# Performance work log

Measured on AMD Instinct MI355X. Metric: run time of the kernel, lower is better.

Reference implementation:

```python
import jax, jax.numpy as jnp
import numpy as np

B, FIN, FOUT, N_TASKS = 256, 1024, 512, 20
FOUT2 = 2 * FOUT  # ConditionalLinear is built with 2*fout


def setup_inputs() -> dict:
    key = jax.random.key(0)
    k1, k2, k3 = jax.random.split(key, 3)
    x = jax.random.normal(k1, (B, FIN), dtype=jnp.float32)
    task_id = jax.random.randint(k2, (B,), 0, N_TASKS)
    # Embedding table [n_tasks, fin*2*fout]; kaiming_normal(fan_out) std = sqrt(2/fout2)
    std = np.sqrt(2.0 / FOUT2).astype(np.float32)
    W = jax.random.normal(k3, (N_TASKS, FIN * FOUT2), dtype=jnp.float32) * std
    return {"x": x, "task_id": task_id, "W": W}


def reference(x, task_id, W):
    Bsz, fin = x.shape
    fout2 = W.shape[1] // fin
    # task-conditional weight gather: [B, 2*fout, fin]
    w = W[task_id].reshape(Bsz, fout2, fin)
    # per-sample matvec (torch.bmm with x.unsqueeze(2))
    logits = jnp.einsum('boi,bi->bo', w, x).reshape(Bsz, fout2 // 2, 2)
    # BinaryGumbelSoftmax eval path: h = 1 - argmax(softmax(logits)) = 1 - argmax(logits)
    h = 1.0 - jnp.argmax(logits, axis=-1).astype(logits.dtype)
    return (h, logits)
```

## Files before the change

kernel.cpp:

```cpp
#include <hip/hip_runtime.h>

#define FIN   1024
#define FOUT2 1024
#define NTASK 20
#define BSZ   256
#define HOFF  (256 * 512)

__global__ __launch_bounds__(256, 2)
void cond_linear_kernel(const float* __restrict__ x,
                        const int* __restrict__ task_id,
                        const float* __restrict__ W,
                        float* __restrict__ out) {
    __shared__ int sh_ord[BSZ];
    __shared__ int wcnt[4];
    __shared__ int sh_n;

    const int tid  = threadIdx.x;
    const int lane = tid & 63;
    const int wv   = tid >> 6;
    const int t    = blockIdx.x >> 6;
    const int tile = blockIdx.x & 63;
    const int o0   = tile * 16 + wv * 4;

    const int my_task = task_id[tid];
    const bool match = (my_task == t);
    const unsigned long long m64 = __ballot(match);
    if (lane == 0) wcnt[wv] = __popcll(m64);
    __syncthreads();
    int base = 0;
    #pragma unroll
    for (int w = 0; w < 4; ++w)
        if (w < wv) base += wcnt[w];
    if (match) {
        const int pos = base + __popcll(m64 & ((1ull << lane) - 1ull));
        sh_ord[pos] = tid;
    }
    if (tid == 0) sh_n = wcnt[0] + wcnt[1] + wcnt[2] + wcnt[3];
    __syncthreads();
    const int n = sh_n;
    if (n == 0) return;

    const float* Wt = W + (size_t)t * (FOUT2 * FIN);
    float4 wr[4][4];
    #pragma unroll
    for (int r = 0; r < 4; ++r) {
        const float4* wp = (const float4*)(Wt + (size_t)(o0 + r) * FIN);
        #pragma unroll
        for (int p = 0; p < 4; ++p)
            wr[r][p] = wp[p * 64 + lane];
    }
    #pragma unroll
    for (int r = 0; r < 4; ++r)
        #pragma unroll
        for (int p = 0; p < 4; ++p)
            asm volatile("" : "+v"(wr[r][p].x), "+v"(wr[r][p].y),
                              "+v"(wr[r][p].z), "+v"(wr[r][p].w));

    int sa = sh_ord[0];
    int sb = sh_ord[(n > 1) ? 1 : 0];
    float4 xa[4], xb[4];
    #pragma unroll
    for (int p = 0; p < 4; ++p)
        xa[p] = ((const float4*)(x + (size_t)sa * FIN))[p * 64 + lane];
    #pragma unroll
    for (int p = 0; p < 4; ++p)
        xb[p] = ((const float4*)(x + (size_t)sb * FIN))[p * 64 + lane];

    for (int i = 0; i + 1 < n; i += 2) {
        const int ia2 = (i + 2 < n) ? i + 2 : i;
        const int ib2 = (i + 3 < n) ? i + 3 : ia2;
        const int na_s = sh_ord[ia2];
        const int nb_s = sh_ord[ib2];
        float4 na[4], nb[4];
        #pragma unroll
        for (int p = 0; p < 4; ++p)
            na[p] = ((const float4*)(x + (size_t)na_s * FIN))[p * 64 + lane];
        #pragma unroll
        for (int p = 0; p < 4; ++p)
            nb[p] = ((const float4*)(x + (size_t)nb_s * FIN))[p * 64 + lane];

        float a0 = 0.f, a1 = 0.f, a2 = 0.f, a3 = 0.f;
        float b0 = 0.f, b1 = 0.f, b2 = 0.f, b3 = 0.f;
        #pragma unroll
        for (int p = 0; p < 4; ++p) {
            const float4 u = xa[p];
            const float4 v = xb[p];
            a0 += wr[0][p].x * u.x + wr[0][p].y * u.y + wr[0][p].z * u.z + wr[0][p].w * u.w;
            a1 += wr[1][p].x * u.x + wr[1][p].y * u.y + wr[1][p].z * u.z + wr[1][p].w * u.w;
            a2 += wr[2][p].x * u.x + wr[2][p].y * u.y + wr[2][p].z * u.z + wr[2][p].w * u.w;
            a3 += wr[3][p].x * u.x + wr[3][p].y * u.y + wr[3][p].z * u.z + wr[3][p].w * u.w;
            b0 += wr[0][p].x * v.x + wr[0][p].y * v.y + wr[0][p].z * v.z + wr[0][p].w * v.w;
            b1 += wr[1][p].x * v.x + wr[1][p].y * v.y + wr[1][p].z * v.z + wr[1][p].w * v.w;
            b2 += wr[2][p].x * v.x + wr[2][p].y * v.y + wr[2][p].z * v.z + wr[2][p].w * v.w;
            b3 += wr[3][p].x * v.x + wr[3][p].y * v.y + wr[3][p].z * v.z + wr[3][p].w * v.w;
        }

        #pragma unroll
        for (int sh = 32; sh >= 1; sh >>= 1) {
            a0 += __shfl_xor(a0, sh, 64);
            a1 += __shfl_xor(a1, sh, 64);
            a2 += __shfl_xor(a2, sh, 64);
            a3 += __shfl_xor(a3, sh, 64);
            b0 += __shfl_xor(b0, sh, 64);
            b1 += __shfl_xor(b1, sh, 64);
            b2 += __shfl_xor(b2, sh, 64);
            b3 += __shfl_xor(b3, sh, 64);
        }
        if (lane == 0) {
            float* la = out + HOFF + (size_t)sa * FOUT2 + o0;
            la[0] = a0; la[1] = a1; la[2] = a2; la[3] = a3;
            out[(size_t)sa * (FOUT2 / 2) + (o0 >> 1)]     = (a0 >= a1) ? 1.0f : 0.0f;
            out[(size_t)sa * (FOUT2 / 2) + (o0 >> 1) + 1] = (a2 >= a3) ? 1.0f : 0.0f;
            float* lb = out + HOFF + (size_t)sb * FOUT2 + o0;
            lb[0] = b0; lb[1] = b1; lb[2] = b2; lb[3] = b3;
            out[(size_t)sb * (FOUT2 / 2) + (o0 >> 1)]     = (b0 >= b1) ? 1.0f : 0.0f;
            out[(size_t)sb * (FOUT2 / 2) + (o0 >> 1) + 1] = (b2 >= b3) ? 1.0f : 0.0f;
        }

        sa = na_s; sb = nb_s;
        #pragma unroll
        for (int p = 0; p < 4; ++p) { xa[p] = na[p]; xb[p] = nb[p]; }
    }

    if (n & 1) {
        float a0 = 0.f, a1 = 0.f, a2 = 0.f, a3 = 0.f;
        #pragma unroll
        for (int p = 0; p < 4; ++p) {
            const float4 u = xa[p];
            a0 += wr[0][p].x * u.x + wr[0][p].y * u.y + wr[0][p].z * u.z + wr[0][p].w * u.w;
            a1 += wr[1][p].x * u.x + wr[1][p].y * u.y + wr[1][p].z * u.z + wr[1][p].w * u.w;
            a2 += wr[2][p].x * u.x + wr[2][p].y * u.y + wr[2][p].z * u.z + wr[2][p].w * u.w;
            a3 += wr[3][p].x * u.x + wr[3][p].y * u.y + wr[3][p].z * u.z + wr[3][p].w * u.w;
        }
        #pragma unroll
        for (int sh = 32; sh >= 1; sh >>= 1) {
            a0 += __shfl_xor(a0, sh, 64);
            a1 += __shfl_xor(a1, sh, 64);
            a2 += __shfl_xor(a2, sh, 64);
            a3 += __shfl_xor(a3, sh, 64);
        }
        if (lane == 0) {
            float* la = out + HOFF + (size_t)sa * FOUT2 + o0;
            la[0] = a0; la[1] = a1; la[2] = a2; la[3] = a3;
            out[(size_t)sa * (FOUT2 / 2) + (o0 >> 1)]     = (a0 >= a1) ? 1.0f : 0.0f;
            out[(size_t)sa * (FOUT2 / 2) + (o0 >> 1) + 1] = (a2 >= a3) ? 1.0f : 0.0f;
        }
    }
}

extern "C" void kernel_launch(void* const* d_in, const int* in_sizes, int n_in,
                              void* d_out, int out_size, void* d_ws, size_t ws_size,
                              hipStream_t stream) {
    const float* x       = (const float*)d_in[0];
    const int*   task_id = (const int*)d_in[1];
    const float* W       = (const float*)d_in[2];
    float*       out     = (float*)d_out;

    dim3 grid(NTASK * 64);
    dim3 block(BSZ);
    hipLaunchKernelGGL(cond_linear_kernel, grid, block, 0, stream,
                       x, task_id, W, out);
}
```

Measured before the change: 35.57 us.

## Split each task's samples across two blocks and use a transposed butterfly reduction

The grid is doubled so that two blocks handle each (task, output tile) pair. Each block processes half of that task's matching samples, which shortens the serial per-block loop over samples. The cross-lane reduction now uses a transpose-style butterfly that folds the 8 partial sums into one value per 8-lane group, so far fewer shuffles are needed, and those lanes write outputs in parallel. An odd sample count is handled by computing the last sample twice instead of in a separate tail. The cost is that each weight tile is read by two blocks, so weight traffic doubles unless the second read hits in cache.

```diff
diff --git a/kernel.cpp b/kernel.cpp
--- a/kernel.cpp
+++ b/kernel.cpp
@@ -18,8 +18,11 @@
     const int tid  = threadIdx.x;
     const int lane = tid & 63;
     const int wv   = tid >> 6;
-    const int t    = blockIdx.x >> 6;
-    const int tile = blockIdx.x & 63;
+    const int bx   = blockIdx.x;
+    const int t    = bx >> 7;
+    const int rem  = bx & 127;
+    const int tile = rem & 63;
+    const int slot = rem >> 6;
     const int o0   = tile * 16 + wv * 4;
 
     const int my_task = task_id[tid];
@@ -38,7 +41,10 @@
     if (tid == 0) sh_n = wcnt[0] + wcnt[1] + wcnt[2] + wcnt[3];
     __syncthreads();
     const int n = sh_n;
-    if (n == 0) return;
+    const int half = (n + 1) >> 1;
+    const int i0 = slot ? half : 0;
+    const int i1 = slot ? n    : half;
+    if (i0 >= i1) return;
 
     const float* Wt = W + (size_t)t * (FOUT2 * FIN);
     float4 wr[4][4];
@@ -56,8 +62,12 @@
             asm volatile("" : "+v"(wr[r][p].x), "+v"(wr[r][p].y),
                               "+v"(wr[r][p].z), "+v"(wr[r][p].w));
 
-    int sa = sh_ord[0];
-    int sb = sh_ord[(n > 1) ? 1 : 0];
+    const bool hi32 = (lane & 32) != 0;
+    const bool hi16 = (lane & 16) != 0;
+    const bool hi8  = (lane & 8)  != 0;
+
+    int sa = sh_ord[i0];
+    int sb = sh_ord[(i0 + 1 < i1) ? i0 + 1 : i1 - 1];
     float4 xa[4], xb[4];
     #pragma unroll
     for (int p = 0; p < 4; ++p)
@@ -66,11 +76,11 @@
     for (int p = 0; p < 4; ++p)
         xb[p] = ((const float4*)(x + (size_t)sb * FIN))[p * 64 + lane];
 
-    for (int i = 0; i + 1 < n; i += 2) {
-        const int ia2 = (i + 2 < n) ? i + 2 : i;
-        const int ib2 = (i + 3 < n) ? i + 3 : ia2;
-        const int na_s = sh_ord[ia2];
-        const int nb_s = sh_ord[ib2];
+    for (int i = i0; i < i1; i += 2) {
+        const int ina = (i + 2 < i1) ? i + 2 : i1 - 1;
+        const int inb = (i + 3 < i1) ? i + 3 : i1 - 1;
+        const int na_s = sh_ord[ina];
+        const int nb_s = sh_ord[inb];
         float4 na[4], nb[4];
         #pragma unroll
         for (int p = 0; p < 4; ++p)
@@ -95,56 +105,45 @@
             b3 += wr[3][p].x * v.x + wr[3][p].y * v.y + wr[3][p].z * v.z + wr[3][p].w * v.w;
         }
 
-        #pragma unroll
-        for (int sh = 32; sh >= 1; sh >>= 1) {
-            a0 += __shfl_xor(a0, sh, 64);
-            a1 += __shfl_xor(a1, sh, 64);
-            a2 += __shfl_xor(a2, sh, 64);
-            a3 += __shfl_xor(a3, sh, 64);
-            b0 += __shfl_xor(b0, sh, 64);
-            b1 += __shfl_xor(b1, sh, 64);
-            b2 += __shfl_xor(b2, sh, 64);
-            b3 += __shfl_xor(b3, sh, 64);
-        }
-        if (lane == 0) {
-            float* la = out + HOFF + (size_t)sa * FOUT2 + o0;
-            la[0] = a0; la[1] = a1; la[2] = a2; la[3] = a3;
-            out[(size_t)sa * (FOUT2 / 2) + (o0 >> 1)]     = (a0 >= a1) ? 1.0f : 0.0f;
-            out[(size_t)sa * (FOUT2 / 2) + (o0 >> 1) + 1] = (a2 >= a3) ? 1.0f : 0.0f;
-            float* lb = out + HOFF + (size_t)sb * FOUT2 + o0;
-            lb[0] = b0; lb[1] = b1; lb[2] = b2; lb[3] = b3;
-            out[(size_t)sb * (FOUT2 / 2) + (o0 >> 1)]     = (b0 >= b1) ? 1.0f : 0.0f;
-            out[(size_t)sb * (FOUT2 / 2) + (o0 >> 1) + 1] = (b2 >= b3) ? 1.0f : 0.0f;
+        const float t0 = a0 + __shfl_xor(a0, 32, 64);
+        const float t1 = a1 + __shfl_xor(a1, 32, 64);
+        const float t2 = a2 + __shfl_xor(a2, 32, 64);
+        const float t3 = a3 + __shfl_xor(a3, 32, 64);
+        const float t4 = b0 + __shfl_xor(b0, 32, 64);
+        const float t5 = b1 + __shfl_xor(b1, 32, 64);
+        const float t6 = b2 + __shfl_xor(b2, 32, 64);
+        const float t7 = b3 + __shfl_xor(b3, 32, 64);
+        float w0 = hi32 ? t4 : t0;
+        float w1 = hi32 ? t5 : t1;
+        float w2 = hi32 ? t6 : t2;
+        float w3 = hi32 ? t7 : t3;
+        w0 += __shfl_xor(w0, 16, 64);
+        w1 += __shfl_xor(w1, 16, 64);
+        w2 += __shfl_xor(w2, 16, 64);
+        w3 += __shfl_xor(w3, 16, 64);
+        float u0 = hi16 ? w2 : w0;
+        float u1 = hi16 ? w3 : w1;
+        u0 += __shfl_xor(u0, 8, 64);
+        u1 += __shfl_xor(u1, 8, 64);
+        float z = hi8 ? u1 : u0;
+        z += __shfl_xor(z, 4, 64);
+        z += __shfl_xor(z, 2, 64);
+        z += __shfl_xor(z, 1, 64);
+        const float zp = __shfl_xor(z, 8, 64);
+
+        const int r_id = (hi8 ? 1 : 0) + (hi16 ? 2 : 0);
+        const int s_idx = hi32 ? sb : sa;
+        if ((lane & 7) == 0) {
+            out[HOFF + (size_t)s_idx * FOUT2 + o0 + r_id] = z;
+            if (!hi8) {
+                out[(size_t)s_idx * (FOUT2 / 2) + (o0 >> 1) + (hi16 ? 1 : 0)]
+                    = (z >= zp) ? 1.0f : 0.0f;
+            }
         }
 
         sa = na_s; sb = nb_s;
         #pragma unroll
         for (int p = 0; p < 4; ++p) { xa[p] = na[p]; xb[p] = nb[p]; }
-    }
-
-    if (n & 1) {
-        float a0 = 0.f, a1 = 0.f, a2 = 0.f, a3 = 0.f;
-        #pragma unroll
-        for (int p = 0; p < 4; ++p) {
-            const float4 u = xa[p];
-            a0 += wr[0][p].x * u.x + wr[0][p].y * u.y + wr[0][p].z * u.z + wr[0][p].w * u.w;
-            a1 += wr[1][p].x * u.x + wr[1][p].y * u.y + wr[1][p].z * u.z + wr[1][p].w * u.w;
-            a2 += wr[2][p].x * u.x + wr[2][p].y * u.y + wr[2][p].z * u.z + wr[2][p].w * u.w;
-            a3 += wr[3][p].x * u.x + wr[3][p].y * u.y + wr[3][p].z * u.z + wr[3][p].w * u.w;
-        }
-        #pragma unroll
-        for (int sh = 32; sh >= 1; sh >>= 1) {
-            a0 += __shfl_xor(a0, sh, 64);
-            a1 += __shfl_xor(a1, sh, 64);
-            a2 += __shfl_xor(a2, sh, 64);
-            a3 += __shfl_xor(a3, sh, 64);
-        }
-        if (lane == 0) {
-            float* la = out + HOFF + (size_t)sa * FOUT2 + o0;
-            la[0] = a0; la[1] = a1; la[2] = a2; la[3] = a3;
-            out[(size_t)sa * (FOUT2 / 2) + (o0 >> 1)]     = (a0 >= a1) ? 1.0f : 0.0f;
-            out[(size_t)sa * (FOUT2 / 2) + (o0 >> 1) + 1] = (a2 >= a3) ? 1.0f : 0.0f;
-        }
     }
 }
 
@@ -156,7 +155,7 @@
     const float* W       = (const float*)d_in[2];
     float*       out     = (float*)d_out;
 
-    dim3 grid(NTASK * 64);
+    dim3 grid(NTASK * 64 * 2);
     dim3 block(BSZ);
     hipLaunchKernelGGL(cond_linear_kernel, grid, block, 0, stream,
                        x, task_id, W, out);
```

New measurement: 31.60 us. 1.13x faster.
